# Kernel optimization log

Hardware: AMD Instinct MI355X
Metric: run time of the kernel (lower is better)

Reference implementation:

```python
import jax, jax.numpy as jnp
import numpy as np

CHANNELS = 512
NUM_HEADS = 4
GROUPS = 32
EPS = 1e-5


def setup_inputs() -> dict:
    key = jax.random.key(0)
    ks = jax.random.split(key, 7)
    C = CHANNELS
    x = jax.random.normal(ks[0], (16, C, 32, 32), dtype=jnp.float32)
    norm_w = jnp.ones((C,), dtype=jnp.float32)
    norm_b = jnp.zeros((C,), dtype=jnp.float32)
    qkv_w = jax.random.normal(ks[1], (3 * C, C), dtype=jnp.float32) * (C ** -0.5)
    qkv_b = jnp.zeros((3 * C,), dtype=jnp.float32)
    proj_w = jax.random.normal(ks[2], (C, C), dtype=jnp.float32) * (C ** -0.5)
    proj_b = jnp.zeros((C,), dtype=jnp.float32)
    return {"x": x, "norm_w": norm_w, "norm_b": norm_b,
            "qkv_w": qkv_w, "qkv_b": qkv_b,
            "proj_w": proj_w, "proj_b": proj_b}


def reference(x, norm_w, norm_b, qkv_w, qkv_b, proj_w, proj_b):
    B, C, H, W = x.shape
    heads = NUM_HEADS
    hd = C // heads  # head dim
    N = H * W

    # GroupNorm(32, C): normalize over (C/32, H, W) per group, then per-channel affine
    xg = x.reshape(B, GROUPS, -1)
    mu = jnp.mean(xg, axis=-1, keepdims=True)
    var = jnp.var(xg, axis=-1, keepdims=True)
    h = ((xg - mu) * jax.lax.rsqrt(var + EPS)).reshape(B, C, H, W)
    h = h * norm_w[None, :, None, None] + norm_b[None, :, None, None]

    # 1x1 conv qkv: [B,C,H,W] -> [B,3C,H,W]
    qkv = jnp.einsum('oc,bchw->bohw', qkv_w, h) + qkv_b[None, :, None, None]
    qkv = qkv.reshape(B, 3, heads, hd, N)
    q, k, v = qkv[:, 0], qkv[:, 1], qkv[:, 2]  # each [B, heads, hd, N]

    scale = hd ** -0.5
    attn = jnp.einsum('bhcn,bhcm->bhnm', q, k) * scale  # [B, heads, N, N]
    attn = jax.nn.softmax(attn, axis=-1)
    h = jnp.einsum('bhnm,bhcm->bhcn', attn, v).reshape(B, C, H, W)

    # 1x1 conv proj + residual
    h = jnp.einsum('oc,bchw->bohw', proj_w, h) + proj_b[None, :, None, None]
    return x + h
```

## Files before the change

kernel.cpp:

```cpp
#include <hip/hip_runtime.h>

typedef __bf16 v8bf __attribute__((ext_vector_type(8)));
typedef float  v4f  __attribute__((ext_vector_type(4)));
typedef unsigned short u16;

__device__ __forceinline__ u16 f2bf(float f){
  __bf16 h = (__bf16)f;
  union { __bf16 h; u16 u; } c; c.h = h; return c.u;
}
__device__ __forceinline__ v4f v4zero(){ v4f z; z[0]=0.f; z[1]=0.f; z[2]=0.f; z[3]=0.f; return z; }

#define MFMA16(a,b,c) __builtin_amdgcn_mfma_f32_16x16x32_bf16((a),(b),(c),0,0,0)

__device__ __forceinline__ void gl_lds16(const u16* g, u16* l){
  __builtin_amdgcn_global_load_lds((const __attribute__((address_space(1))) void*)g,
                                   (__attribute__((address_space(3))) void*)l, 16, 0, 0);
}

__global__ __launch_bounds__(256) void cvt2_kernel(const float* __restrict__ a, u16* __restrict__ da, int na,
                                                   const float* __restrict__ b, u16* __restrict__ db, int nb){
  int i = (blockIdx.x*256 + threadIdx.x)*4;
  const float* s; u16* d; int off;
  if (i < na){ s = a; d = da; off = i; }
  else { off = i - na; if (off >= nb) return; s = b; d = db; }
  float4 v = *(const float4*)(s + off);
  ushort4 o;
  o.x = f2bf(v.x); o.y = f2bf(v.y); o.z = f2bf(v.z); o.w = f2bf(v.w);
  *(ushort4*)(d + off) = o;
}

__global__ __launch_bounds__(256) void gn_fused_kernel(const float* __restrict__ x, const float* __restrict__ nw,
                                                       const float* __restrict__ nb, u16* __restrict__ h_t){
  __shared__ float xs[16*1028 + 16];
  const int bg = blockIdx.x, b = bg >> 5, g = bg & 31, c0 = g*16;
  const int tid = threadIdx.x;
  const float* base = x + (size_t)(b*512 + c0)*1024;

  float s = 0.f, ss = 0.f;
  #pragma unroll
  for (int it = 0; it < 16; ++it){
    float4 v = *(const float4*)(base + it*1024 + tid*4);
    s  += v.x + v.y + v.z + v.w;
    ss += v.x*v.x + v.y*v.y + v.z*v.z + v.w*v.w;
    *(float4*)(xs + it*1028 + tid*4) = v;
  }
  #pragma unroll
  for (int off = 32; off > 0; off >>= 1){ s += __shfl_down(s, off); ss += __shfl_down(ss, off); }
  float* red = xs + 16*1028;
  int w = tid >> 6;
  if ((tid & 63) == 0){ red[w] = s; red[4+w] = ss; }
  __syncthreads();
  if (tid == 0){
    float S  = red[0]+red[1]+red[2]+red[3];
    float SS = red[4]+red[5]+red[6]+red[7];
    float mean = S * (1.f/16384.f);
    float var  = SS * (1.f/16384.f) - mean*mean;
    red[8] = mean;
    red[9] = rsqrtf(var + 1e-5f);
  }
  __syncthreads();
  const float mean = red[8], rstd = red[9];

  const int half = tid & 1, nbase = tid >> 1;
  float wv[8], bv[8];
  #pragma unroll
  for (int cl = 0; cl < 8; ++cl){
    int c = c0 + half*8 + cl;
    wv[cl] = nw[c] * rstd;
    bv[cl] = nb[c] - mean * wv[cl];
  }
  #pragma unroll
  for (int p = 0; p < 8; ++p){
    int n = nbase + p*128;
    alignas(16) u16 tmp[8];
    #pragma unroll
    for (int cl = 0; cl < 8; ++cl)
      tmp[cl] = f2bf(xs[(half*8 + cl)*1028 + n] * wv[cl] + bv[cl]);
    *(int4*)(h_t + ((size_t)b*1024 + n)*512 + c0 + half*8) = *(int4*)tmp;
  }
}

__global__ __launch_bounds__(256,2) void gemm_qkv_kernel(
    const u16* __restrict__ A,
    const u16* __restrict__ B,
    const float* __restrict__ bias,
    u16* __restrict__ qk_t, u16* __restrict__ v_ws)
{
  __shared__ u16 smem[24576];
  const int tid = threadIdx.x, w = tid>>6, lane = tid&63, col = lane&15, quad = lane>>4;
  const int m0 = blockIdx.y*128;
  const int n0 = blockIdx.x*256;
  const int b  = blockIdx.z;
  const int lr = lane>>2;
  const int gsw = ((lane&3) ^ (lr&3))*8;
  const u16* Ag = A + ((size_t)b*1024 + m0 + w*32 + lr)*512 + gsw;
  const u16* Bg = B + (size_t)(n0 + w*64 + lr)*512 + gsw;
  const int mw = (w&1)*64, nw = (w>>1)*128;
  const int fsw = (quad ^ (col&3))*8;

  v4f acc[4][8];
  #pragma unroll
  for (int i=0;i<4;++i)
    #pragma unroll
    for (int j=0;j<8;++j) acc[i][j] = v4zero();

  {
    u16* Ab = smem + (w*32)*32;
    u16* Bb = smem + 4096 + (w*64)*32;
    #pragma unroll
    for (int p = 0; p < 2; ++p) gl_lds16(Ag + (size_t)(p*16)*512, Ab + p*512);
    #pragma unroll
    for (int p = 0; p < 4; ++p) gl_lds16(Bg + (size_t)(p*16)*512, Bb + p*512);
  }

  for (int kt = 0; kt < 16; ++kt){
    __syncthreads();
    if (kt < 15){
      u16* Ab = smem + ((kt+1)&1)*12288 + (w*32)*32;
      u16* Bb = smem + ((kt+1)&1)*12288 + 4096 + (w*64)*32;
      int ko = (kt+1)*32;
      #pragma unroll
      for (int p = 0; p < 2; ++p) gl_lds16(Ag + (size_t)(p*16)*512 + ko, Ab + p*512);
      #pragma unroll
      for (int p = 0; p < 4; ++p) gl_lds16(Bg + (size_t)(p*16)*512 + ko, Bb + p*512);
    }
    const u16* As = smem + (kt&1)*12288;
    const u16* Bs = As + 4096;
    v8bf a[4], bb[8];
    #pragma unroll
    for (int i = 0; i < 4; ++i) a[i]  = *(const v8bf*)(As + (mw+i*16+col)*32 + fsw);
    #pragma unroll
    for (int j = 0; j < 8; ++j) bb[j] = *(const v8bf*)(Bs + (nw+j*16+col)*32 + fsw);
    #pragma unroll
    for (int i = 0; i < 4; ++i)
      #pragma unroll
      for (int j = 0; j < 8; ++j)
        acc[i][j] = MFMA16(a[i], bb[j], acc[i][j]);
  }
  __syncthreads();

  float bc[8];
  #pragma unroll
  for (int j = 0; j < 8; ++j)
    bc[j] = bias[n0 + nw + j*16 + col];

  if (n0 < 1024){
    u16* Cs = smem + w*(64*72);
    #pragma unroll
    for (int half = 0; half < 2; ++half){
      #pragma unroll
      for (int i = 0; i < 4; ++i)
        #pragma unroll
        for (int jj = 0; jj < 4; ++jj)
          #pragma unroll
          for (int r = 0; r < 4; ++r)
            Cs[(i*16+quad*4+r)*72 + jj*16+col] = f2bf(acc[i][half*4+jj][r] + bc[half*4+jj]);
      u16* dst = qk_t + (size_t)b*1024*1024;
      #pragma unroll
      for (int p = 0; p < 8; ++p){
        int rl = p*8 + (lane>>3), cl = (lane&7)*8;
        *(int4*)(dst + (size_t)(m0+mw+rl)*1024 + n0+nw+half*64+cl) = *(int4*)(Cs + rl*72 + cl);
      }
    }
  } else {
    u16* Ct = smem + w*(64*80);
    #pragma unroll
    for (int half = 0; half < 2; ++half){
      #pragma unroll
      for (int i = 0; i < 4; ++i)
        #pragma unroll
        for (int jj = 0; jj < 4; ++jj)
          #pragma unroll
          for (int r = 0; r < 4; ++r)
            Ct[(jj*16+col)*80 + i*16+quad*4+r] = f2bf(acc[i][half*4+jj][r] + bc[half*4+jj]);
      u16* dst = v_ws + (size_t)b*512*1024;
      #pragma unroll
      for (int p = 0; p < 8; ++p){
        int rl = p*8 + (lane>>3), cl = (lane&7)*8;
        *(int4*)(dst + (size_t)(n0-1024 + nw + half*64 + rl)*1024 + m0+mw+cl) = *(int4*)(Ct + rl*80 + cl);
      }
    }
  }
}

__global__ __launch_bounds__(256,2) void gemm_bt_kernel(
    const u16* __restrict__ A, long long sA,
    const u16* __restrict__ B, long long sB,
    u16* __restrict__ Cbf, float* __restrict__ Cf, long long sC,
    const float* __restrict__ bias_row,
    const float* __restrict__ bias_col,
    const float* __restrict__ residf, long long sR,
    int M, int N, int K)
{
  __shared__ u16 smem[32768];
  const int tid = threadIdx.x, w = tid>>6, lane = tid&63, col = lane&15, quad = lane>>4;
  const int m0 = blockIdx.y*128, n0 = blockIdx.x*128;
  const int lr8 = lane>>3;
  const int gsw = ((lane&7) ^ lr8)*8;
  const u16* Ag = A + (size_t)blockIdx.z*sA + (size_t)(m0 + w*32 + lr8)*K + gsw;
  const u16* Bg = B + (size_t)blockIdx.z*sB + (size_t)(n0 + w*32 + lr8)*K + gsw;
  const int mw = (w&1)*64, nw = (w>>1)*64;
  const int csw = col&7;
  const int nt = K >> 6;

  v4f acc[4][4];
  #pragma unroll
  for (int i=0;i<4;++i)
    #pragma unroll
    for (int j=0;j<4;++j) acc[i][j] = v4zero();

  {
    u16* Ab = smem + (w*32)*64;
    u16* Bb = smem + 8192 + (w*32)*64;
    #pragma unroll
    for (int p = 0; p < 4; ++p){
      gl_lds16(Ag + (size_t)(p*8)*K, Ab + p*512);
      gl_lds16(Bg + (size_t)(p*8)*K, Bb + p*512);
    }
  }

  for (int kt = 0; kt < nt; ++kt){
    __syncthreads();
    if (kt+1 < nt){
      u16* Ab = smem + ((kt+1)&1)*16384 + (w*32)*64;
      u16* Bb = smem + ((kt+1)&1)*16384 + 8192 + (w*32)*64;
      int ko = (kt+1)*64;
      #pragma unroll
      for (int p = 0; p < 4; ++p){
        gl_lds16(Ag + (size_t)(p*8)*K + ko, Ab + p*512);
        gl_lds16(Bg + (size_t)(p*8)*K + ko, Bb + p*512);
      }
    }
    const u16* As = smem + (kt&1)*16384;
    const u16* Bs = As + 8192;
    #pragma unroll
    for (int kh = 0; kh < 2; ++kh){
      const int fs = ((kh*4 + quad) ^ csw)*8;
      v8bf a[4], bb[4];
      #pragma unroll
      for (int i = 0; i < 4; ++i) a[i]  = *(const v8bf*)(As + (mw+i*16+col)*64 + fs);
      #pragma unroll
      for (int j = 0; j < 4; ++j) bb[j] = *(const v8bf*)(Bs + (nw+j*16+col)*64 + fs);
      #pragma unroll
      for (int i = 0; i < 4; ++i)
        #pragma unroll
        for (int j = 0; j < 4; ++j)
          acc[i][j] = MFMA16(a[i], bb[j], acc[i][j]);
    }
  }
  __syncthreads();

  float br[4][4], bc[4];
  #pragma unroll
  for (int i = 0; i < 4; ++i)
    #pragma unroll
    for (int r = 0; r < 4; ++r)
      br[i][r] = bias_row ? bias_row[m0+mw+i*16+quad*4+r] : 0.f;
  #pragma unroll
  for (int j = 0; j < 4; ++j)
    bc[j] = bias_col ? bias_col[n0+nw+j*16+col] : 0.f;

  if (Cf){
    float* Cb = Cf + (size_t)blockIdx.z*sC;
    const float* Rb = residf ? residf + (size_t)blockIdx.z*sR : nullptr;
    #pragma unroll
    for (int i = 0; i < 4; ++i)
      #pragma unroll
      for (int r = 0; r < 4; ++r){
        int row = m0+mw+i*16+quad*4+r;
        #pragma unroll
        for (int j = 0; j < 4; ++j){
          size_t goff = (size_t)row*N + n0+nw+j*16+col;
          float val = acc[i][j][r] + br[i][r] + bc[j];
          if (Rb) val += Rb[goff];
          Cb[goff] = val;
        }
      }
  } else {
    u16* Cs = smem + w*(64*72);
    #pragma unroll
    for (int i = 0; i < 4; ++i)
      #pragma unroll
      for (int j = 0; j < 4; ++j)
        #pragma unroll
        for (int r = 0; r < 4; ++r)
          Cs[(i*16+quad*4+r)*72 + j*16+col] = f2bf(acc[i][j][r] + br[i][r] + bc[j]);
    __syncthreads();
    u16* Cb = Cbf + (size_t)blockIdx.z*sC;
    #pragma unroll
    for (int p = 0; p < 8; ++p){
      int rl = p*8 + (lane>>3), cl = (lane&7)*8;
      size_t goff = (size_t)(m0+mw+rl)*N + n0+nw+cl;
      *(int4*)(Cb + goff) = *(int4*)(Cs + rl*72 + cl);
    }
  }
}

__global__ __launch_bounds__(256,2) void attn_kernel(const u16* __restrict__ qk, const u16* __restrict__ vv,
                                                     u16* __restrict__ outp){
  __shared__ u16 smem[40960];
  u16* Ks = smem;
  u16* Vs = smem + 16384;
  u16* Ps = smem + 32768;
  const int id = blockIdx.x;
  const int qt = id >> 6, bh = id & 63, b = bh >> 2, h = bh & 3;
  const int n0 = qt*128;
  const int tid = threadIdx.x, w = tid>>6, lane = tid&63, col = lane&15, quad = lane>>4;
  const size_t bq = (size_t)b*1024*1024;
  const float scale2 = 0.12751742f;

  v8bf aq[2][4];
  #pragma unroll
  for (int i = 0; i < 2; ++i)
    #pragma unroll
    for (int kk = 0; kk < 4; ++kk)
      aq[i][kk] = *(const v8bf*)(qk + bq + (size_t)(n0 + w*32 + i*16 + col)*1024 + h*128 + kk*32 + quad*8);

  v4f o[2][8];
  #pragma unroll
  for (int i=0;i<2;++i)
    #pragma unroll
    for (int j=0;j<8;++j) o[i][j] = v4zero();
  float lsum[8];
  #pragma unroll
  for (int r=0;r<8;++r) lsum[r] = 0.f;

  const int krow = w*4 + (lane>>4);
  const int kgr  = (lane&15) ^ (krow&7);
  const u16* kg_base = qk + bq + (size_t)krow*1024 + 512 + h*128 + kgr*8;
  const int vrow = w*8 + (lane>>3);
  const int vgr  = (lane&7) ^ (vrow&7);
  const u16* vg_base = vv + ((size_t)b*512 + h*128 + vrow)*1024 + vgr*8;

  #pragma unroll
  for (int p = 0; p < 4; ++p)
    gl_lds16(kg_base + (size_t)(p*16)*1024, Ks + (w*4)*128 + p*2048);
  #pragma unroll
  for (int p = 0; p < 4; ++p)
    gl_lds16(vg_base + (size_t)(p*32)*1024, Vs + (w*8)*64 + p*2048);

  for (int t = 0; t < 16; ++t){
    const int mt = t*64;
    __syncthreads();

    if (t < 15){
      int mt2 = mt + 64;
      u16* kl = Ks + (((t+1)&1)<<13) + (w*4)*128;
      #pragma unroll
      for (int p = 0; p < 4; ++p)
        gl_lds16(kg_base + (size_t)(mt2 + p*16)*1024, kl + p*2048);
      u16* vl = Vs + (((t+1)&1)<<13) + (w*8)*64;
      #pragma unroll
      for (int p = 0; p < 4; ++p)
        gl_lds16(vg_base + (size_t)(p*32)*1024 + mt2, vl + p*2048);
    }

    const u16* Kc = Ks + ((t&1)<<13);
    v4f s[2][4];
    #pragma unroll
    for (int i=0;i<2;++i)
      #pragma unroll
      for (int j=0;j<4;++j) s[i][j] = v4zero();
    #pragma unroll
    for (int kk = 0; kk < 4; ++kk){
      v8bf bk[4];
      #pragma unroll
      for (int j = 0; j < 4; ++j){
        int r = j*16 + col;
        int g = (kk*4 + quad) ^ (r&7);
        bk[j] = *(const v8bf*)(Kc + (r<<7) + (g<<3));
      }
      #pragma unroll
      for (int i = 0; i < 2; ++i)
        #pragma unroll
        for (int j = 0; j < 4; ++j)
          s[i][j] = MFMA16(aq[i][kk], bk[j], s[i][j]);
    }

    #pragma unroll
    for (int i = 0; i < 2; ++i)
      #pragma unroll
      for (int r = 0; r < 4; ++r){
        int rr = w*32 + i*16 + quad*4 + r;
        int key = (rr ^ (rr>>2)) & 7;
        int rbase = (rr<<6) + (col&7);
        float ps[4];
        #pragma unroll
        for (int j = 0; j < 4; ++j){
          float pv = __builtin_amdgcn_exp2f(s[i][j][r]*scale2);
          ps[j] = pv;
          Ps[rbase + ((((j*16+col)>>3) ^ key)<<3)] = f2bf(pv);
        }
        lsum[i*4+r] += (ps[0]+ps[1]) + (ps[2]+ps[3]);
      }

    const u16* Vc = Vs + ((t&1)<<13);
    #pragma unroll
    for (int kk = 0; kk < 2; ++kk){
      v8bf ap[2];
      #pragma unroll
      for (int i = 0; i < 2; ++i){
        int rr = w*32 + i*16 + col;
        int key = (rr ^ (rr>>2)) & 7;
        int g = (kk*4 + quad) ^ key;
        ap[i] = *(const v8bf*)(Ps + (rr<<6) + (g<<3));
      }
      #pragma unroll
      for (int j = 0; j < 8; ++j){
        int vr = j*16 + col;
        int g = (kk*4 + quad) ^ (vr&7);
        v8bf bv = *(const v8bf*)(Vc + (vr<<6) + (g<<3));
        #pragma unroll
        for (int i = 0; i < 2; ++i) o[i][j] = MFMA16(ap[i], bv, o[i][j]);
      }
    }
  }
  __syncthreads();

  #pragma unroll
  for (int i = 0; i < 2; ++i)
    #pragma unroll
    for (int r = 0; r < 4; ++r){
      float l = lsum[i*4+r];
      l += __shfl_xor(l, 1);
      l += __shfl_xor(l, 2);
      l += __shfl_xor(l, 4);
      l += __shfl_xor(l, 8);
      float inv = 1.f / l;
      #pragma unroll
      for (int j = 0; j < 8; ++j) o[i][j][r] *= inv;
    }

  #pragma unroll
  for (int i = 0; i < 2; ++i)
    #pragma unroll
    for (int j = 0; j < 8; ++j)
      #pragma unroll
      for (int r = 0; r < 4; ++r){
        int rr = w*32 + i*16 + quad*4 + r;
        int c  = j*16 + col;
        smem[(rr<<7) + ((((c>>3) ^ (rr&7))<<3)) + (c&7)] = f2bf(o[i][j][r]);
      }
  __syncthreads();
  #pragma unroll
  for (int p = 0; p < 8; ++p){
    int nr = p*16 + (tid>>4);
    int gc = (tid&15) ^ (nr&7);
    *(int4*)(outp + ((size_t)b*1024 + n0 + nr)*512 + h*128 + ((tid&15)<<3)) =
      *(int4*)(smem + (nr<<7) + (gc<<3));
  }
}

extern "C" void kernel_launch(void* const* d_in, const int* in_sizes, int n_in,
                              void* d_out, int out_size, void* d_ws, size_t ws_size,
                              hipStream_t stream){
  const float* x      = (const float*)d_in[0];
  const float* norm_w = (const float*)d_in[1];
  const float* norm_b = (const float*)d_in[2];
  const float* qkv_w  = (const float*)d_in[3];
  const float* qkv_b  = (const float*)d_in[4];
  const float* proj_w = (const float*)d_in[5];
  const float* proj_b = (const float*)d_in[6];
  float* out = (float*)d_out;

  u16* h_t   = (u16*)d_ws;
  u16* qk_t  = h_t  + (size_t)16*1024*512;
  u16* v_ws  = qk_t + (size_t)16*1024*1024;
  u16* wq_bf = v_ws + (size_t)16*512*1024;
  u16* wp_bf = wq_bf + (size_t)1536*512;
  u16* attnout = h_t;

  cvt2_kernel<<<1024, 256, 0, stream>>>(qkv_w, wq_bf, 1536*512, proj_w, wp_bf, 512*512);
  gn_fused_kernel<<<512, 256, 0, stream>>>(x, norm_w, norm_b, h_t);

  gemm_qkv_kernel<<<dim3(6,8,16), 256, 0, stream>>>(h_t, wq_bf, qkv_b, qk_t, v_ws);

  attn_kernel<<<512, 256, 0, stream>>>(qk_t, v_ws, attnout);

  gemm_bt_kernel<<<dim3(8,4,16), 256, 0, stream>>>(
      wp_bf, 0, attnout, (long long)1024*512,
      nullptr, out, (long long)512*1024, proj_b, nullptr, x, (long long)512*1024, 512, 1024, 512);
}
```

Before: 211.3 us.

## Compute transposed S with 32x32 MFMA and keep P in registers

Rewrites the attention inner loop to use 32x32x16 bf16 MFMAs that compute S transposed (keys x queries), so each lane holds probabilities for one query column. P is packed to bf16 with v_cvt_pk_bf16_f32 and rearranged across half-waves with v_permlane32_swap, then fed directly as the A operand of the PV MFMA. This removes the LDS round trip for P and its shared-memory buffer. It also adds s_setprio around the MFMA bursts. The trade-off is more register pressure and a reliance on exact lane-layout assumptions for the permlane swap and the final row-sum shuffle.

```diff
diff --git a/kernel.cpp b/kernel.cpp
--- a/kernel.cpp
+++ b/kernel.cpp
@@ -2,6 +2,7 @@
 
 typedef __bf16 v8bf __attribute__((ext_vector_type(8)));
 typedef float  v4f  __attribute__((ext_vector_type(4)));
+typedef float  v16f __attribute__((ext_vector_type(16)));
 typedef unsigned short u16;
 
 __device__ __forceinline__ u16 f2bf(float f){
@@ -11,10 +12,17 @@
 __device__ __forceinline__ v4f v4zero(){ v4f z; z[0]=0.f; z[1]=0.f; z[2]=0.f; z[3]=0.f; return z; }
 
 #define MFMA16(a,b,c) __builtin_amdgcn_mfma_f32_16x16x32_bf16((a),(b),(c),0,0,0)
+#define MFMA32(a,b,c) __builtin_amdgcn_mfma_f32_32x32x16_bf16((a),(b),(c),0,0,0)
 
 __device__ __forceinline__ void gl_lds16(const u16* g, u16* l){
   __builtin_amdgcn_global_load_lds((const __attribute__((address_space(1))) void*)g,
                                    (__attribute__((address_space(3))) void*)l, 16, 0, 0);
+}
+
+__device__ __forceinline__ unsigned int pkbf(float lo, float hi){
+  unsigned int r;
+  asm("v_cvt_pk_bf16_f32 %0, %1, %2" : "=v"(r) : "v"(lo), "v"(hi));
+  return r;
 }
 
 __global__ __launch_bounds__(256) void cvt2_kernel(const float* __restrict__ a, u16* __restrict__ da, int na,
@@ -298,32 +306,32 @@
 
 __global__ __launch_bounds__(256,2) void attn_kernel(const u16* __restrict__ qk, const u16* __restrict__ vv,
                                                      u16* __restrict__ outp){
-  __shared__ u16 smem[40960];
+  __shared__ u16 smem[32768];
   u16* Ks = smem;
   u16* Vs = smem + 16384;
-  u16* Ps = smem + 32768;
   const int id = blockIdx.x;
   const int qt = id >> 6, bh = id & 63, b = bh >> 2, h = bh & 3;
   const int n0 = qt*128;
-  const int tid = threadIdx.x, w = tid>>6, lane = tid&63, col = lane&15, quad = lane>>4;
+  const int tid = threadIdx.x, w = tid>>6, lane = tid&63;
+  const int nl = lane & 31, hi = lane >> 5;
+  const int key = nl & 7;
   const size_t bq = (size_t)b*1024*1024;
   const float scale2 = 0.12751742f;
 
-  v8bf aq[2][4];
-  #pragma unroll
-  for (int i = 0; i < 2; ++i)
-    #pragma unroll
-    for (int kk = 0; kk < 4; ++kk)
-      aq[i][kk] = *(const v8bf*)(qk + bq + (size_t)(n0 + w*32 + i*16 + col)*1024 + h*128 + kk*32 + quad*8);
-
-  v4f o[2][8];
-  #pragma unroll
-  for (int i=0;i<2;++i)
-    #pragma unroll
-    for (int j=0;j<8;++j) o[i][j] = v4zero();
-  float lsum[8];
-  #pragma unroll
-  for (int r=0;r<8;++r) lsum[r] = 0.f;
+  v8bf qf[8];
+  {
+    const u16* qbase = qk + bq + (size_t)(n0 + w*32 + nl)*1024 + h*128 + hi*8;
+    #pragma unroll
+    for (int kk = 0; kk < 8; ++kk)
+      qf[kk] = *(const v8bf*)(qbase + kk*16);
+  }
+
+  v16f o[4];
+  #pragma unroll
+  for (int j=0;j<4;++j)
+    #pragma unroll
+    for (int r=0;r<16;++r) o[j][r] = 0.f;
+  float lsum = 0.f;
 
   const int krow = w*4 + (lane>>4);
   const int kgr  = (lane&15) ^ (krow&7);
@@ -356,91 +364,72 @@
     }
 
     const u16* Kc = Ks + ((t&1)<<13);
-    v4f s[2][4];
-    #pragma unroll
-    for (int i=0;i<2;++i)
-      #pragma unroll
-      for (int j=0;j<4;++j) s[i][j] = v4zero();
-    #pragma unroll
-    for (int kk = 0; kk < 4; ++kk){
-      v8bf bk[4];
-      #pragma unroll
-      for (int j = 0; j < 4; ++j){
-        int r = j*16 + col;
-        int g = (kk*4 + quad) ^ (r&7);
-        bk[j] = *(const v8bf*)(Kc + (r<<7) + (g<<3));
+    v16f s0, s1;
+    #pragma unroll
+    for (int r=0;r<16;++r){ s0[r]=0.f; s1[r]=0.f; }
+    __builtin_amdgcn_s_setprio(1);
+    #pragma unroll
+    for (int kk = 0; kk < 8; ++kk){
+      int g = (((kk*2 + hi) ^ key) << 3);
+      v8bf k0 = *(const v8bf*)(Kc + (nl<<7) + g);
+      v8bf k1 = *(const v8bf*)(Kc + ((32+nl)<<7) + g);
+      s0 = MFMA32(k0, qf[kk], s0);
+      s1 = MFMA32(k1, qf[kk], s1);
+    }
+    __builtin_amdgcn_s_setprio(0);
+
+    #pragma unroll
+    for (int r = 0; r < 16; ++r){
+      s0[r] = __builtin_amdgcn_exp2f(s0[r]*scale2);
+      s1[r] = __builtin_amdgcn_exp2f(s1[r]*scale2);
+      lsum += s0[r] + s1[r];
+    }
+
+    const u16* Vc = Vs + ((t&1)<<13);
+    #pragma unroll
+    for (int half = 0; half < 2; ++half){
+      const v16f& ps = half ? s1 : s0;
+      #pragma unroll
+      for (int sel = 0; sel < 2; ++sel){
+        const int sb = sel*8;
+        unsigned int pA = pkbf(ps[sb+0], ps[sb+1]);
+        unsigned int pB = pkbf(ps[sb+2], ps[sb+3]);
+        unsigned int pC = pkbf(ps[sb+4], ps[sb+5]);
+        unsigned int pD = pkbf(ps[sb+6], ps[sb+7]);
+        asm("v_permlane32_swap_b32 %0, %1" : "+v"(pA), "+v"(pC));
+        asm("v_permlane32_swap_b32 %0, %1" : "+v"(pB), "+v"(pD));
+        union { v8bf v; unsigned int u[4]; } pa;
+        pa.u[0] = pA; pa.u[1] = pB; pa.u[2] = pC; pa.u[3] = pD;
+        const int kkv = half*2 + sel;
+        const int gv = (((kkv*2 + hi) ^ key) << 3);
+        __builtin_amdgcn_s_setprio(1);
+        #pragma unroll
+        for (int j = 0; j < 4; ++j){
+          v8bf bv = *(const v8bf*)(Vc + ((j*32 + nl)<<6) + gv);
+          o[j] = MFMA32(pa.v, bv, o[j]);
+        }
+        __builtin_amdgcn_s_setprio(0);
       }
-      #pragma unroll
-      for (int i = 0; i < 2; ++i)
-        #pragma unroll
-        for (int j = 0; j < 4; ++j)
-          s[i][j] = MFMA16(aq[i][kk], bk[j], s[i][j]);
-    }
-
-    #pragma unroll
-    for (int i = 0; i < 2; ++i)
-      #pragma unroll
-      for (int r = 0; r < 4; ++r){
-        int rr = w*32 + i*16 + quad*4 + r;
-        int key = (rr ^ (rr>>2)) & 7;
-        int rbase = (rr<<6) + (col&7);
-        float ps[4];
-        #pragma unroll
-        for (int j = 0; j < 4; ++j){
-          float pv = __builtin_amdgcn_exp2f(s[i][j][r]*scale2);
-          ps[j] = pv;
-          Ps[rbase + ((((j*16+col)>>3) ^ key)<<3)] = f2bf(pv);
-        }
-        lsum[i*4+r] += (ps[0]+ps[1]) + (ps[2]+ps[3]);
-      }
-
-    const u16* Vc = Vs + ((t&1)<<13);
-    #pragma unroll
-    for (int kk = 0; kk < 2; ++kk){
-      v8bf ap[2];
-      #pragma unroll
-      for (int i = 0; i < 2; ++i){
-        int rr = w*32 + i*16 + col;
-        int key = (rr ^ (rr>>2)) & 7;
-        int g = (kk*4 + quad) ^ key;
-        ap[i] = *(const v8bf*)(Ps + (rr<<6) + (g<<3));
-      }
-      #pragma unroll
-      for (int j = 0; j < 8; ++j){
-        int vr = j*16 + col;
-        int g = (kk*4 + quad) ^ (vr&7);
-        v8bf bv = *(const v8bf*)(Vc + (vr<<6) + (g<<3));
-        #pragma unroll
-        for (int i = 0; i < 2; ++i) o[i][j] = MFMA16(ap[i], bv, o[i][j]);
-      }
-    }
-  }
-  __syncthreads();
-
-  #pragma unroll
-  for (int i = 0; i < 2; ++i)
-    #pragma unroll
-    for (int r = 0; r < 4; ++r){
-      float l = lsum[i*4+r];
-      l += __shfl_xor(l, 1);
-      l += __shfl_xor(l, 2);
-      l += __shfl_xor(l, 4);
-      l += __shfl_xor(l, 8);
-      float inv = 1.f / l;
-      #pragma unroll
-      for (int j = 0; j < 8; ++j) o[i][j][r] *= inv;
-    }
-
-  #pragma unroll
-  for (int i = 0; i < 2; ++i)
-    #pragma unroll
-    for (int j = 0; j < 8; ++j)
-      #pragma unroll
-      for (int r = 0; r < 4; ++r){
-        int rr = w*32 + i*16 + quad*4 + r;
-        int c  = j*16 + col;
-        smem[(rr<<7) + ((((c>>3) ^ (rr&7))<<3)) + (c&7)] = f2bf(o[i][j][r]);
-      }
+    }
+  }
+  __syncthreads();
+
+  lsum += __shfl_xor(lsum, 32);
+  float invl[16];
+  #pragma unroll
+  for (int r = 0; r < 16; ++r){
+    int nr = (r&3) + 8*(r>>2) + 4*hi;
+    invl[r] = 1.f / __shfl(lsum, nr);
+  }
+
+  #pragma unroll
+  for (int j = 0; j < 4; ++j)
+    #pragma unroll
+    for (int r = 0; r < 16; ++r){
+      int rr = w*32 + (r&3) + 8*(r>>2) + 4*hi;
+      int c  = j*32 + nl;
+      smem[(rr<<7) + ((((c>>3) ^ (rr&7))<<3)) + (c&7)] = f2bf(o[j][r] * invl[r]);
+    }
   __syncthreads();
   #pragma unroll
   for (int p = 0; p < 8; ++p){
```

Measured after the change: 206.9 us. -2.1%, faster.
